# Performance work log

Hardware: AMD Instinct MI355X
Metric: run time of the kernel (lower is better)

Reference implementation:

```python
import jax, jax.numpy as jnp
import numpy as np

GN_EPS = 1e-5
NN_EPS = 1e-8


def _three_nn_interpolate(xyz1, xyz2, points2):
    # xyz1: (B,N,3), xyz2: (B,M,3), points2: (B,M,C) -> (B,N,C)
    src_sq = jnp.sum(xyz1 ** 2, axis=-1, keepdims=True)          # (B,N,1)
    dst_sq = jnp.sum(xyz2 ** 2, axis=-1)[:, None, :]             # (B,1,M)
    inner = jnp.einsum('bnd,bmd->bnm', xyz1, xyz2)               # (B,N,M)
    dist = src_sq - 2.0 * inner + dst_sq                         # (B,N,M)
    neg_d, idx = jax.lax.top_k(-dist, 3)                         # (B,N,3)
    d = -neg_d
    inv = 1.0 / (d + NN_EPS)
    w = inv / jnp.sum(inv, axis=-1, keepdims=True)               # (B,N,3)
    grouped = jax.vmap(lambda p, i: p[i])(points2, idx)          # (B,N,3,C)
    return jnp.sum(grouped * w[..., None], axis=2)               # (B,N,C)


def _group_norm(x, weight, bias, groups):
    # x: (B,C,N)
    B, C, N = x.shape
    xg = x.reshape(B, groups, C // groups, N)
    mu = jnp.mean(xg, axis=(2, 3), keepdims=True)
    var = jnp.var(xg, axis=(2, 3), keepdims=True)
    xg = (xg - mu) * jax.lax.rsqrt(var + GN_EPS)
    x = xg.reshape(B, C, N)
    return x * weight[None, :, None] + bias[None, :, None]


def setup_inputs() -> dict:
    key = jax.random.key(0)
    ks = jax.random.split(key, 10)
    B, N, M, C1, C2 = 8, 8192, 2048, 128, 256
    mlp = [256, 128]
    in_ch = C1 + C2
    inp = {
        'xyz1': jax.random.normal(ks[0], (B, N, 3), dtype=jnp.float32),
        'xyz2': jax.random.normal(ks[1], (B, M, 3), dtype=jnp.float32),
        'points1': jax.random.normal(ks[2], (B, N, C1), dtype=jnp.float32),
        'points2': jax.random.normal(ks[3], (B, M, C2), dtype=jnp.float32),
        'w0': jax.random.normal(ks[4], (mlp[0], in_ch), dtype=jnp.float32) * (1.0 / np.sqrt(in_ch)),
        'w1': jax.random.normal(ks[5], (mlp[1], mlp[0]), dtype=jnp.float32) * (1.0 / np.sqrt(mlp[0])),
        'gn0_w': jnp.ones((mlp[0],), dtype=jnp.float32),
        'gn0_b': jnp.zeros((mlp[0],), dtype=jnp.float32),
        'gn1_w': jnp.ones((mlp[1],), dtype=jnp.float32),
        'gn1_b': jnp.zeros((mlp[1],), dtype=jnp.float32),
    }
    return inp


def reference(xyz1, xyz2, points1, points2, w0, w1, gn0_w, gn0_b, gn1_w, gn1_b):
    interpolated = _three_nn_interpolate(xyz1, xyz2, points2)    # (B,N,C2)
    feat = jnp.concatenate([points1, interpolated], axis=-1)     # (B,N,C1+C2)
    # conv1d kernel size 1 == pointwise matmul; work in (B,C,N) layout for GN
    h = jnp.einsum('bnc,oc->bon', feat, w0)                      # (B,256,N)
    h = jax.nn.relu(_group_norm(h, gn0_w, gn0_b, groups=min(32, w0.shape[0])))
    h = jnp.einsum('bcn,oc->bon', h, w1)                         # (B,128,N)
    h = jax.nn.relu(_group_norm(h, gn1_w, gn1_b, groups=min(32, w1.shape[0])))
    return jnp.transpose(h, (0, 2, 1))                           # (B,N,128)
```

## Files before the change

### kernel.cpp

```cpp
#include <hip/hip_runtime.h>


#define DEVI __device__ __forceinline__

static constexpr int B  = 8;
static constexpr int N  = 8192;
static constexpr int M  = 2048;
static constexpr int C1 = 128;
static constexpr int C2 = 256;
static constexpr int CIN = C1 + C2;
static constexpr int H0 = 256;
static constexpr int H1 = 128;
static constexpr int BN = B * N;
static constexpr int NSEG = 8;
static constexpr int SEGL = M / NSEG;

typedef __bf16 bf16x8 __attribute__((ext_vector_type(8)));
typedef float  f32x4  __attribute__((ext_vector_type(4)));
typedef unsigned short ushort8v __attribute__((ext_vector_type(8)));

DEVI float bf2f(unsigned short u) {
    union { unsigned int i; float f; } v; v.i = ((unsigned int)u) << 16; return v.f;
}
DEVI unsigned short f2bf(float f) {
    union { float f; unsigned int i; } v; v.f = f;
    unsigned int x = v.i;
    return (unsigned short)((x + 0x7fffu + ((x >> 16) & 1u)) >> 16);
}
DEVI float ldin(const void* p, size_t i, int bf) {
    return bf ? bf2f(((const unsigned short*)p)[i]) : ((const float*)p)[i];
}
DEVI void ld8(const void* p, size_t i, int bf, float r[8]) {
    if (bf) {
        const ushort8v u = *(const ushort8v*)((const unsigned short*)p + i);
#pragma unroll
        for (int k = 0; k < 8; k++) r[k] = bf2f(u[k]);
    } else {
        const float4 a = *(const float4*)((const float*)p + i);
        const float4 b = *(const float4*)((const float*)p + i + 4);
        r[0] = a.x; r[1] = a.y; r[2] = a.z; r[3] = a.w;
        r[4] = b.x; r[5] = b.y; r[6] = b.z; r[7] = b.w;
    }
}

DEVI void gload16(const void* g, void* l) {
    __builtin_amdgcn_global_load_lds(
        (const __attribute__((address_space(1))) void*)g,
        (__attribute__((address_space(3))) void*)l, 16, 0, 0);
}

__global__ __launch_bounds__(64) void detect_dtype_kernel(const void* __restrict__ xyz1,
                                                          int* __restrict__ flag)
{
    const unsigned short* u = (const unsigned short*)xyz1;
    const int lane = threadIdx.x;
    const float av = fabsf(bf2f(u[2 * lane]));
    const bool in_range = (av >= 1e-4f && av <= 100.0f);
    const unsigned long long m = __ballot(in_range);
    if (lane == 0) flag[0] = (__popcll(m) >= 32) ? 1 : 0;
}

__global__ __launch_bounds__(256) void prep_kernel(
    const void* __restrict__ w0, const void* __restrict__ w1,
    const void* __restrict__ xyz2,
    unsigned short* __restrict__ w0b, unsigned short* __restrict__ w1b,
    float4* __restrict__ c4, float* __restrict__ partz,
    const int* __restrict__ flag)
{
    const int bf = flag[0];
    const int n0 = H0 * CIN;
    const int n1 = H1 * H0;
    const int n2 = B * M;
    const int n3 = 1024;
    const int total = n0 + n1 + n2 + n3;
    for (int i = blockIdx.x * blockDim.x + threadIdx.x; i < total; i += gridDim.x * blockDim.x) {
        if (i < n0) {
            w0b[i] = bf ? ((const unsigned short*)w0)[i] : f2bf(((const float*)w0)[i]);
        } else if (i < n0 + n1) {
            const int j = i - n0;
            w1b[j] = bf ? ((const unsigned short*)w1)[j] : f2bf(((const float*)w1)[j]);
        } else if (i < n0 + n1 + n2) {
            const int j = i - n0 - n1;
            const float x = ldin(xyz2, (size_t)j * 3 + 0, bf);
            const float y = ldin(xyz2, (size_t)j * 3 + 1, bf);
            const float z = ldin(xyz2, (size_t)j * 3 + 2, bf);
            const float sq = __fadd_rn(__fadd_rn(__fmul_rn(x, x), __fmul_rn(y, y)), __fmul_rn(z, z));
            c4[j] = make_float4(x, y, z, 0.5f * sq);
        } else {
            partz[i - n0 - n1 - n2] = 0.f;
        }
    }
}

__global__ __launch_bounds__(256) void knn3_split_kernel(
    const void* __restrict__ xyz1, const float4* __restrict__ c4,
    int* __restrict__ ci, const int* __restrict__ flag)
{
    const int bf = flag[0];
    const int tid = threadIdx.x;
    const int gid = blockIdx.x * 256 + tid;
    const int s = blockIdx.y;
    const int b = __builtin_amdgcn_readfirstlane(gid >> 13);

    const float x1 = ldin(xyz1, (size_t)gid * 3 + 0, bf);
    const float y1 = ldin(xyz1, (size_t)gid * 3 + 1, bf);
    const float z1 = ldin(xyz1, (size_t)gid * 3 + 2, bf);

    const float4* __restrict__ cand = c4 + b * M + s * SEGL;
    const int jbase = s * SEGL;
    constexpr int HALF = SEGL / 2;

    float a0 = 3.4e38f, a1 = 3.4e38f, a2 = 3.4e38f;
    int   ia0 = 0, ia1 = 0, ia2 = 0;
    float g0 = 3.4e38f, g1 = 3.4e38f, g2 = 3.4e38f;
    int   ig0 = 0, ig1 = 0, ig2 = 0;

#pragma unroll 4
    for (int j = 0; j < HALF; ++j) {
        const float4 pA = cand[j];
        const float4 pB = cand[j + HALF];
        const float sA = __builtin_fmaf(-x1, pA.x,
                          __builtin_fmaf(-y1, pA.y,
                           __builtin_fmaf(-z1, pA.z, pA.w)));
        const float sB = __builtin_fmaf(-x1, pB.x,
                          __builtin_fmaf(-y1, pB.y,
                           __builtin_fmaf(-z1, pB.z, pB.w)));
        {
            const int jn = jbase + j;
            const bool c0 = sA < a0;
            const float t1 = fmaxf(sA, a0); a0 = fminf(sA, a0);
            const int  tj1 = c0 ? ia0 : jn; ia0 = c0 ? jn : ia0;
            const bool c1 = t1 < a1;
            const float t2 = fmaxf(t1, a1); a1 = fminf(t1, a1);
            const int  tj2 = c1 ? ia1 : tj1; ia1 = c1 ? tj1 : ia1;
            const bool c2 = t2 < a2;
            a2 = fminf(t2, a2); ia2 = c2 ? tj2 : ia2;
        }
        {
            const int jn = jbase + HALF + j;
            const bool c0 = sB < g0;
            const float t1 = fmaxf(sB, g0); g0 = fminf(sB, g0);
            const int  tj1 = c0 ? ig0 : jn; ig0 = c0 ? jn : ig0;
            const bool c1 = t1 < g1;
            const float t2 = fmaxf(t1, g1); g1 = fminf(t1, g1);
            const int  tj2 = c1 ? ig1 : tj1; ig1 = c1 ? tj1 : ig1;
            const bool c2 = t2 < g2;
            g2 = fminf(t2, g2); ig2 = c2 ? tj2 : ig2;
        }
    }

    float mv[3] = { g0, g1, g2 };
    int   mi[3] = { ig0, ig1, ig2 };
#pragma unroll
    for (int k = 0; k < 3; ++k) {
        const float sv = mv[k]; const int jn = mi[k];
        const bool c0 = sv < a0;
        const float t1 = fmaxf(sv, a0); a0 = fminf(sv, a0);
        const int  tj1 = c0 ? ia0 : jn; ia0 = c0 ? jn : ia0;
        const bool c1 = t1 < a1;
        const float t2 = fmaxf(t1, a1); a1 = fminf(t1, a1);
        const int  tj2 = c1 ? ia1 : tj1; ia1 = c1 ? tj1 : ia1;
        const bool c2 = t2 < a2;
        a2 = fminf(t2, a2); ia2 = c2 ? tj2 : ia2;
    }

    ci[(size_t)(s * 3 + 0) * BN + gid] = ia0;
    ci[(size_t)(s * 3 + 1) * BN + gid] = ia1;
    ci[(size_t)(s * 3 + 2) * BN + gid] = ia2;
}

__global__ __launch_bounds__(256) void knn3_merge_kernel(
    const void* __restrict__ xyz1, const float4* __restrict__ c4,
    const int* __restrict__ ci,
    int* __restrict__ nn_idx, float* __restrict__ nn_w,
    const int* __restrict__ flag)
{
    const int bf = flag[0];
    const int gid = blockIdx.x * 256 + threadIdx.x;
    const int b = gid >> 13;

    const float x1 = ldin(xyz1, (size_t)gid * 3 + 0, bf);
    const float y1 = ldin(xyz1, (size_t)gid * 3 + 1, bf);
    const float z1 = ldin(xyz1, (size_t)gid * 3 + 2, bf);
    const float sq1 = __fadd_rn(__fadd_rn(__fmul_rn(x1, x1), __fmul_rn(y1, y1)), __fmul_rn(z1, z1));

    float bd0 = 3.4e38f, bd1 = 3.4e38f, bd2 = 3.4e38f;
    int   bi0 = 0x7fffffff, bi1 = 0x7fffffff, bi2 = 0x7fffffff;

#pragma unroll
    for (int k = 0; k < 3 * NSEG; ++k) {
        const int ix = ci[(size_t)k * BN + gid];
        const float4 p = c4[b * M + ix];
        const float inner = __fadd_rn(__fadd_rn(__fmul_rn(x1, p.x), __fmul_rn(y1, p.y)),
                                      __fmul_rn(z1, p.z));
        const float pw2 = p.w + p.w;
        const float d = __fadd_rn(__fsub_rn(sq1, __fmul_rn(2.0f, inner)), pw2);
        const bool lt2 = (d < bd2) || (d == bd2 && ix < bi2);
        if (lt2) {
            const bool lt0 = (d < bd0) || (d == bd0 && ix < bi0);
            const bool lt1 = (d < bd1) || (d == bd1 && ix < bi1);
            if (lt0)      { bd2 = bd1; bi2 = bi1; bd1 = bd0; bi1 = bi0; bd0 = d; bi0 = ix; }
            else if (lt1) { bd2 = bd1; bi2 = bi1; bd1 = d; bi1 = ix; }
            else          { bd2 = d; bi2 = ix; }
        }
    }

    const float v0 = 1.0f / (bd0 + 1e-8f);
    const float v1 = 1.0f / (bd1 + 1e-8f);
    const float v2 = 1.0f / (bd2 + 1e-8f);
    const float s = v0 + v1 + v2;
    nn_idx[gid * 3 + 0] = bi0; nn_idx[gid * 3 + 1] = bi1; nn_idx[gid * 3 + 2] = bi2;
    nn_w[gid * 3 + 0] = v0 / s; nn_w[gid * 3 + 1] = v1 / s; nn_w[gid * 3 + 2] = v2 / s;
}

__global__ __launch_bounds__(256, 2) void gemm1_kernel(
    const void* __restrict__ p1, const void* __restrict__ p2,
    const int* __restrict__ nn_idx, const float* __restrict__ nn_w,
    const unsigned short* __restrict__ W,
    unsigned short* __restrict__ h0, float2* __restrict__ part,
    const int* __restrict__ flag)
{
    constexpr int K = CIN;
    constexpr int COUT = H0;
    __shared__ __align__(16) char lds[49152];

    const int bf = flag[0];
    const int tid = threadIdx.x;
    const int l   = tid & 63;
    const int w   = tid >> 6;
    const int rowBase = blockIdx.x * 128;
    const int b = rowBase >> 13;

    const int srow  = l >> 3;
    const int sslot = l & 7;

    int arow[4]; int aidx[4][3]; float aw[4][3];
#pragma unroll
    for (int i = 0; i < 4; i++) {
        const int r = (w * 4 + i) * 8 + srow;
        arow[i] = r;
        const int p = rowBase + r;
#pragma unroll
        for (int k = 0; k < 3; k++) {
            aidx[i][k] = nn_idx[p * 3 + k];
            aw[i][k]   = nn_w[p * 3 + k];
        }
    }

    f32x4 acc[4][8];
#pragma unroll
    for (int i = 0; i < 4; i++)
#pragma unroll
        for (int j = 0; j < 8; j++) acc[i][j] = (f32x4)0.0f;

    const int wr  = (tid >> 7) & 1;
    const int wc  = (tid >> 6) & 1;
    const int rl  = l & 15;
    const int kq  = l >> 4;
    const int swz = (l & 7) << 4;
    int aoff[4], boff[8];
#pragma unroll
    for (int i = 0; i < 4; i++) aoff[i] = (wr * 64 + i * 16 + rl) * 128;
#pragma unroll
    for (int j = 0; j < 8; j++) boff[j] = 16384 + (wc * 128 + j * 16 + rl) * 128;

    constexpr int NT = K / 64;

#pragma unroll 1
    for (int t = 0; t < NT; ++t) {
        const int k0 = t * 64;
#pragma unroll
        for (int i = 0; i < 8; ++i) {
            const int cb = w * 8 + i;
            const int r  = cb * 8 + srow;
            const int ke = (sslot ^ (r & 7)) << 3;
            gload16(W + ((size_t)r * K + k0 + ke), lds + 16384 + cb * 1024);
        }
#pragma unroll
        for (int i = 0; i < 4; ++i) {
            const int r = arow[i];
            const int kslot = sslot ^ (r & 7);
            const int c = k0 + (kslot << 3);
            float v[8];
            if (k0 < C1) {
                ld8(p1, (size_t)(rowBase + r) * C1 + c, bf, v);
            } else {
                const int c2 = c - C1;
                float t0[8], t1[8], t2[8];
                ld8(p2, (size_t)(b * M + aidx[i][0]) * C2 + c2, bf, t0);
                ld8(p2, (size_t)(b * M + aidx[i][1]) * C2 + c2, bf, t1);
                ld8(p2, (size_t)(b * M + aidx[i][2]) * C2 + c2, bf, t2);
                const float w0v = aw[i][0], w1v = aw[i][1], w2v = aw[i][2];
#pragma unroll
                for (int k = 0; k < 8; k++) v[k] = w0v * t0[k] + w1v * t1[k] + w2v * t2[k];
            }
            ushort8v o;
#pragma unroll
            for (int k = 0; k < 8; k++) o[k] = f2bf(v[k]);
            *(ushort8v*)(lds + r * 128 + (sslot << 4)) = o;
        }
        __syncthreads();
#pragma unroll
        for (int ks = 0; ks < 2; ++ks) {
            const int kb = (ks * 64 + kq * 16) ^ swz;
            bf16x8 af[4], bfr[8];
#pragma unroll
            for (int i = 0; i < 4; i++) af[i]  = *(const bf16x8*)(lds + aoff[i] + kb);
#pragma unroll
            for (int j = 0; j < 8; j++) bfr[j] = *(const bf16x8*)(lds + boff[j] + kb);
#pragma unroll
            for (int i = 0; i < 4; i++)
#pragma unroll
                for (int j = 0; j < 8; j++)
                    acc[i][j] = __builtin_amdgcn_mfma_f32_16x16x32_bf16(af[i], bfr[j], acc[i][j], 0, 0, 0);
        }
        __syncthreads();
    }

    const int crow = rowBase + wr * 64 + kq * 4;
    const int ccol = wc * 128 + rl;
    float gsum[8], gss[8];
#pragma unroll
    for (int j = 0; j < 8; j++) {
        float s = 0.f, ss = 0.f;
#pragma unroll
        for (int i = 0; i < 4; i++)
#pragma unroll
            for (int r = 0; r < 4; r++) {
                const unsigned short hb = f2bf(acc[i][j][r]);
                h0[(size_t)(crow + i * 16 + r) * COUT + ccol + j * 16] = hb;
                const float x = bf2f(hb);
                s += x; ss += x * x;
            }
        gsum[j] = s; gss[j] = ss;
    }
    __syncthreads();
    float2* sred = (float2*)lds;
    if (tid < 32) sred[tid] = make_float2(0.f, 0.f);
    __syncthreads();
#pragma unroll
    for (int j = 0; j < 8; j++) {
        const int g = wc * 16 + j * 2 + (rl >> 3);
        atomicAdd(&sred[g].x, gsum[j]);
        atomicAdd(&sred[g].y, gss[j]);
    }
    __syncthreads();
    if (tid < 32) {
        atomicAdd(&part[b * 32 + tid].x, sred[tid].x);
        atomicAdd(&part[b * 32 + tid].y, sred[tid].y);
    }
}

__global__ __launch_bounds__(256) void gemm2_kernel(
    const unsigned short* __restrict__ h0, const float2* __restrict__ st0,
    const void* __restrict__ gw, const void* __restrict__ gb,
    const unsigned short* __restrict__ W,
    unsigned short* __restrict__ h1, float2* __restrict__ part,
    const int* __restrict__ flag)
{
    constexpr int K = H0;
    constexpr int COUT = H1;
    __shared__ __align__(16) char lds[32768];

    const int bf = flag[0];
    const int tid = threadIdx.x;
    const int l   = tid & 63;
    const int w   = tid >> 6;
    const int rowBase = blockIdx.x * 128;
    const int b = rowBase >> 13;

    const int srow  = l >> 3;
    const int sslot = l & 7;

    f32x4 acc[4][4];
#pragma unroll
    for (int i = 0; i < 4; i++)
#pragma unroll
        for (int j = 0; j < 4; j++) acc[i][j] = (f32x4)0.0f;

    const int wr  = (tid >> 7) & 1;
    const int wc  = (tid >> 6) & 1;
    const int rl  = l & 15;
    const int kq  = l >> 4;
    const int swz = (l & 7) << 4;
    int aoff[4], boff[4];
#pragma unroll
    for (int i = 0; i < 4; i++) {
        aoff[i] = (wr * 64 + i * 16 + rl) * 128;
        boff[i] = 16384 + (wc * 64 + i * 16 + rl) * 128;
    }

    constexpr int NT = K / 64;

#pragma unroll 1
    for (int t = 0; t < NT; ++t) {
        const int k0 = t * 64;
#pragma unroll
        for (int i = 0; i < 4; ++i) {
            const int cb = w * 4 + i;
            const int r  = cb * 8 + srow;
            const int ke = (sslot ^ (r & 7)) << 3;
            gload16(W + ((size_t)r * K + k0 + ke), lds + 16384 + cb * 1024);
        }
#pragma unroll
        for (int i = 0; i < 4; ++i) {
            const int r = (w * 4 + i) * 8 + srow;
            const int kslot = sslot ^ (r & 7);
            const int c = k0 + (kslot << 3);
            const float2 ms = st0[b * 32 + (c >> 3)];
            float gwv[8], gbv[8];
            ld8(gw, c, bf, gwv);
            ld8(gb, c, bf, gbv);
            const ushort8v hv = *(const ushort8v*)(h0 + (size_t)(rowBase + r) * H0 + c);
            ushort8v o;
#pragma unroll
            for (int k = 0; k < 8; k++) {
                const float x = bf2f(hv[k]);
                o[k] = f2bf(fmaxf((x - ms.x) * ms.y * gwv[k] + gbv[k], 0.f));
            }
            *(ushort8v*)(lds + r * 128 + (sslot << 4)) = o;
        }
        __syncthreads();
#pragma unroll
        for (int ks = 0; ks < 2; ++ks) {
            const int kb = (ks * 64 + kq * 16) ^ swz;
            bf16x8 af[4], bfr[4];
#pragma unroll
            for (int i = 0; i < 4; i++) af[i]  = *(const bf16x8*)(lds + aoff[i] + kb);
#pragma unroll
            for (int j = 0; j < 4; j++) bfr[j] = *(const bf16x8*)(lds + boff[j] + kb);
#pragma unroll
            for (int i = 0; i < 4; i++)
#pragma unroll
                for (int j = 0; j < 4; j++)
                    acc[i][j] = __builtin_amdgcn_mfma_f32_16x16x32_bf16(af[i], bfr[j], acc[i][j], 0, 0, 0);
        }
        __syncthreads();
    }

    const int crow = rowBase + wr * 64 + kq * 4;
    const int ccol = wc * 64 + rl;
    float gsum[4], gss[4];
#pragma unroll
    for (int j = 0; j < 4; j++) {
        float s = 0.f, ss = 0.f;
#pragma unroll
        for (int i = 0; i < 4; i++)
#pragma unroll
            for (int r = 0; r < 4; r++) {
                const unsigned short hb = f2bf(acc[i][j][r]);
                h1[(size_t)(crow + i * 16 + r) * COUT + ccol + j * 16] = hb;
                const float x = bf2f(hb);
                s += x; ss += x * x;
            }
        gsum[j] = s; gss[j] = ss;
    }
    __syncthreads();
    float2* sred = (float2*)lds;
    if (tid < 32) sred[tid] = make_float2(0.f, 0.f);
    __syncthreads();
#pragma unroll
    for (int j = 0; j < 4; j++) {
        const int g = wc * 16 + j * 4 + (rl >> 2);
        atomicAdd(&sred[g].x, gsum[j]);
        atomicAdd(&sred[g].y, gss[j]);
    }
    __syncthreads();
    if (tid < 32) {
        atomicAdd(&part[b * 32 + tid].x, sred[tid].x);
        atomicAdd(&part[b * 32 + tid].y, sred[tid].y);
    }
}

__global__ __launch_bounds__(256) void gn_finalize_kernel(
    const float2* __restrict__ part, float2* __restrict__ st, float cnt)
{
    const int t = threadIdx.x;
    const float2 p = part[t];
    const float mu  = p.x / cnt;
    const float var = p.y / cnt - mu * mu;
    st[t] = make_float2(mu, rsqrtf(var + 1e-5f));
}

__global__ __launch_bounds__(256) void gn_norm_relu_kernel(
    const unsigned short* __restrict__ h, const float2* __restrict__ st,
    const void* __restrict__ gw, const void* __restrict__ gb,
    void* __restrict__ out, int C, int cpg, int total4,
    const int* __restrict__ flag)
{
    const int bf = flag[0];
    const int C4 = C >> 2;
    for (int i4 = blockIdx.x * blockDim.x + threadIdx.x; i4 < total4; i4 += gridDim.x * blockDim.x) {
        const int c = (i4 % C4) * 4;
        const int p = i4 / C4;
        const int b = p >> 13;
        const float2 ms = st[b * (C / cpg) + c / cpg];
        const ushort4 hv = *(const ushort4*)(h + (size_t)i4 * 4);
        float r[4] = { bf2f(hv.x), bf2f(hv.y), bf2f(hv.z), bf2f(hv.w) };
#pragma unroll
        for (int k = 0; k < 4; k++) {
            const float gwv = ldin(gw, c + k, bf);
            const float gbv = ldin(gb, c + k, bf);
            r[k] = fmaxf((r[k] - ms.x) * ms.y * gwv + gbv, 0.f);
        }
        if (bf) {
            ushort4 o;
            o.x = f2bf(r[0]); o.y = f2bf(r[1]); o.z = f2bf(r[2]); o.w = f2bf(r[3]);
            *(ushort4*)((unsigned short*)out + (size_t)i4 * 4) = o;
        } else {
            float4 o; o.x = r[0]; o.y = r[1]; o.z = r[2]; o.w = r[3];
            *(float4*)((float*)out + (size_t)i4 * 4) = o;
        }
    }
}

extern "C" void kernel_launch(void* const* d_in, const int* in_sizes, int n_in,
                              void* d_out, int out_size, void* d_ws, size_t ws_size,
                              hipStream_t stream)
{
    const void* xyz1    = d_in[0];
    const void* xyz2    = d_in[1];
    const void* points1 = d_in[2];
    const void* points2 = d_in[3];
    const void* w0      = d_in[4];
    const void* w1      = d_in[5];
    const void* gn0w    = d_in[6];
    const void* gn0b    = d_in[7];
    const void* gn1w    = d_in[8];
    const void* gn1b    = d_in[9];

    char* ws = (char*)d_ws;
    int*            nn_idx = (int*)ws;
    float*          nn_w   = (float*)(ws + 786432);
    unsigned short* h0     = (unsigned short*)(ws + 1572864);
    unsigned short* h1     = (unsigned short*)(ws + 35127296);
    unsigned short* w0b    = (unsigned short*)(ws + 51904512);
    unsigned short* w1b    = (unsigned short*)(ws + 52101120);
    float2*         st0    = (float2*)(ws + 52166656);
    float2*         st1    = (float2*)(ws + 52168704);
    int*            flag   = (int*)(ws + 52170752);
    float4*         c4     = (float4*)(ws + 52170816);
    int*            ci     = (int*)(ws + 52432960);
    float2*         part0  = (float2*)(ws + 58724416);
    float2*         part1  = (float2*)(ws + 58726464);

    detect_dtype_kernel<<<1, 64, 0, stream>>>(xyz1, flag);

    prep_kernel<<<576, 256, 0, stream>>>(w0, w1, xyz2, w0b, w1b, c4, (float*)part0, flag);

    {
        dim3 g(BN / 256, NSEG);
        knn3_split_kernel<<<g, 256, 0, stream>>>(xyz1, c4, ci, flag);
    }
    knn3_merge_kernel<<<BN / 256, 256, 0, stream>>>(xyz1, c4, ci, nn_idx, nn_w, flag);

    gemm1_kernel<<<BN / 128, 256, 0, stream>>>(points1, points2, nn_idx, nn_w,
                                               w0b, h0, part0, flag);
    gn_finalize_kernel<<<1, 256, 0, stream>>>(part0, st0, (float)N * (H0 / 32));

    gemm2_kernel<<<BN / 128, 256, 0, stream>>>(h0, st0, gn0w, gn0b, w1b, h1, part1, flag);
    gn_finalize_kernel<<<1, 256, 0, stream>>>(part1, st1, (float)N * (H1 / 32));

    gn_norm_relu_kernel<<<1024, 256, 0, stream>>>(h1, st1, gn1w, gn1b, d_out,
                                                  H1, H1 / 32, BN * H1 / 4, flag);
}
```

Baseline: 353.7 us.

## Split interpolation out of GEMM1 into a bf16 feature buffer and retile GEMM1

Converts points1 and points2 to bf16 in the prep kernel. A new kernel gathers the three neighbours, interpolates them and writes a concatenated bf16 feature matrix. GEMM1 then loads both its A and B tiles through global_load_lds with 512 threads and 4x4 MFMA tiles per wave, instead of doing gathers inside its K loop. This removes the irregular gather latency from the matmul, but adds a round trip of the ~50MB feature buffer through memory and extra conversion traffic.

```diff
diff --git a/kernel.cpp b/kernel.cpp
--- a/kernel.cpp
+++ b/kernel.cpp
@@ -42,6 +42,11 @@
         r[4] = b.x; r[5] = b.y; r[6] = b.z; r[7] = b.w;
     }
 }
+DEVI void ld8b(const unsigned short* p, size_t i, float r[8]) {
+    const ushort8v u = *(const ushort8v*)(p + i);
+#pragma unroll
+    for (int k = 0; k < 8; k++) r[k] = bf2f(u[k]);
+}
 
 DEVI void gload16(const void* g, void* l) {
     __builtin_amdgcn_global_load_lds(
@@ -60,35 +65,56 @@
     if (lane == 0) flag[0] = (__popcll(m) >= 32) ? 1 : 0;
 }
 
+DEVI void cvt8(const void* src, unsigned short* dst, size_t j8, int bf) {
+    if (bf) {
+        *(ushort8v*)(dst + j8 * 8) = *(const ushort8v*)((const unsigned short*)src + j8 * 8);
+    } else {
+        float r[8];
+        ld8(src, j8 * 8, 0, r);
+        ushort8v o;
+#pragma unroll
+        for (int k = 0; k < 8; k++) o[k] = f2bf(r[k]);
+        *(ushort8v*)(dst + j8 * 8) = o;
+    }
+}
+
 __global__ __launch_bounds__(256) void prep_kernel(
     const void* __restrict__ w0, const void* __restrict__ w1,
+    const void* __restrict__ p1, const void* __restrict__ p2,
     const void* __restrict__ xyz2,
     unsigned short* __restrict__ w0b, unsigned short* __restrict__ w1b,
+    unsigned short* __restrict__ pb1, unsigned short* __restrict__ pb2,
     float4* __restrict__ c4, float* __restrict__ partz,
     const int* __restrict__ flag)
 {
     const int bf = flag[0];
-    const int n0 = H0 * CIN;
-    const int n1 = H1 * H0;
-    const int n2 = B * M;
-    const int n3 = 1024;
-    const int total = n0 + n1 + n2 + n3;
-    for (int i = blockIdx.x * blockDim.x + threadIdx.x; i < total; i += gridDim.x * blockDim.x) {
-        if (i < n0) {
-            w0b[i] = bf ? ((const unsigned short*)w0)[i] : f2bf(((const float*)w0)[i]);
-        } else if (i < n0 + n1) {
-            const int j = i - n0;
-            w1b[j] = bf ? ((const unsigned short*)w1)[j] : f2bf(((const float*)w1)[j]);
-        } else if (i < n0 + n1 + n2) {
-            const int j = i - n0 - n1;
+    constexpr int R0 = H0 * CIN / 8;
+    constexpr int R1 = H1 * H0 / 8;
+    constexpr int R2 = B * M;
+    constexpr int R3 = BN * C1 / 8;
+    constexpr int R4 = B * M * C2 / 8;
+    constexpr int R5 = 1024;
+    constexpr int TOT = R0 + R1 + R2 + R3 + R4 + R5;
+    for (int i = blockIdx.x * blockDim.x + threadIdx.x; i < TOT; i += gridDim.x * blockDim.x) {
+        int j = i;
+        if (j < R0) { cvt8(w0, w0b, j, bf); continue; }
+        j -= R0;
+        if (j < R1) { cvt8(w1, w1b, j, bf); continue; }
+        j -= R1;
+        if (j < R2) {
             const float x = ldin(xyz2, (size_t)j * 3 + 0, bf);
             const float y = ldin(xyz2, (size_t)j * 3 + 1, bf);
             const float z = ldin(xyz2, (size_t)j * 3 + 2, bf);
             const float sq = __fadd_rn(__fadd_rn(__fmul_rn(x, x), __fmul_rn(y, y)), __fmul_rn(z, z));
             c4[j] = make_float4(x, y, z, 0.5f * sq);
-        } else {
-            partz[i - n0 - n1 - n2] = 0.f;
-        }
+            continue;
+        }
+        j -= R2;
+        if (j < R3) { cvt8(p1, pb1, j, bf); continue; }
+        j -= R3;
+        if (j < R4) { cvt8(p2, pb2, j, bf); continue; }
+        j -= R4;
+        partz[j] = 0.f;
     }
 }
 
@@ -213,18 +239,47 @@
     nn_w[gid * 3 + 0] = v0 / s; nn_w[gid * 3 + 1] = v1 / s; nn_w[gid * 3 + 2] = v2 / s;
 }
 
-__global__ __launch_bounds__(256, 2) void gemm1_kernel(
-    const void* __restrict__ p1, const void* __restrict__ p2,
+__global__ __launch_bounds__(256) void interp_concat_kernel(
+    const unsigned short* __restrict__ pb1, const unsigned short* __restrict__ pb2,
     const int* __restrict__ nn_idx, const float* __restrict__ nn_w,
+    unsigned short* __restrict__ feat)
+{
+    const int total = BN * (CIN / 8);
+    for (int idx = blockIdx.x * blockDim.x + threadIdx.x; idx < total; idx += gridDim.x * blockDim.x) {
+        const int c8 = idx % 48;
+        const int p  = idx / 48;
+        const int c  = c8 * 8;
+        if (c < C1) {
+            *(ushort8v*)(feat + (size_t)idx * 8) =
+                *(const ushort8v*)(pb1 + (size_t)p * C1 + c);
+        } else {
+            const int b  = p >> 13;
+            const int c2 = c - C1;
+            const int*   id = nn_idx + p * 3;
+            const float* wv = nn_w  + p * 3;
+            float t0[8], t1[8], t2[8];
+            ld8b(pb2, (size_t)(b * M + id[0]) * C2 + c2, t0);
+            ld8b(pb2, (size_t)(b * M + id[1]) * C2 + c2, t1);
+            ld8b(pb2, (size_t)(b * M + id[2]) * C2 + c2, t2);
+            const float w0v = wv[0], w1v = wv[1], w2v = wv[2];
+            ushort8v o;
+#pragma unroll
+            for (int k = 0; k < 8; k++)
+                o[k] = f2bf(w0v * t0[k] + w1v * t1[k] + w2v * t2[k]);
+            *(ushort8v*)(feat + (size_t)idx * 8) = o;
+        }
+    }
+}
+
+__global__ __launch_bounds__(512) void gemm1_kernel(
+    const unsigned short* __restrict__ A,
     const unsigned short* __restrict__ W,
-    unsigned short* __restrict__ h0, float2* __restrict__ part,
-    const int* __restrict__ flag)
+    unsigned short* __restrict__ h0, float2* __restrict__ part)
 {
     constexpr int K = CIN;
     constexpr int COUT = H0;
     __shared__ __align__(16) char lds[49152];
 
-    const int bf = flag[0];
     const int tid = threadIdx.x;
     const int l   = tid & 63;
     const int w   = tid >> 6;
@@ -234,35 +289,23 @@
     const int srow  = l >> 3;
     const int sslot = l & 7;
 
-    int arow[4]; int aidx[4][3]; float aw[4][3];
-#pragma unroll
-    for (int i = 0; i < 4; i++) {
-        const int r = (w * 4 + i) * 8 + srow;
-        arow[i] = r;
-        const int p = rowBase + r;
-#pragma unroll
-        for (int k = 0; k < 3; k++) {
-            aidx[i][k] = nn_idx[p * 3 + k];
-            aw[i][k]   = nn_w[p * 3 + k];
-        }
-    }
-
-    f32x4 acc[4][8];
+    f32x4 acc[4][4];
 #pragma unroll
     for (int i = 0; i < 4; i++)
 #pragma unroll
-        for (int j = 0; j < 8; j++) acc[i][j] = (f32x4)0.0f;
-
-    const int wr  = (tid >> 7) & 1;
-    const int wc  = (tid >> 6) & 1;
+        for (int j = 0; j < 4; j++) acc[i][j] = (f32x4)0.0f;
+
+    const int wr  = w >> 2;
+    const int wc  = w & 3;
     const int rl  = l & 15;
     const int kq  = l >> 4;
     const int swz = (l & 7) << 4;
-    int aoff[4], boff[8];
-#pragma unroll
-    for (int i = 0; i < 4; i++) aoff[i] = (wr * 64 + i * 16 + rl) * 128;
-#pragma unroll
-    for (int j = 0; j < 8; j++) boff[j] = 16384 + (wc * 128 + j * 16 + rl) * 128;
+    int aoff[4], boff[4];
+#pragma unroll
+    for (int i = 0; i < 4; i++) {
+        aoff[i] = (wr * 64 + i * 16 + rl) * 128;
+        boff[i] = 16384 + (wc * 64 + i * 16 + rl) * 128;
+    }
 
     constexpr int NT = K / 64;
 
@@ -270,58 +313,41 @@
     for (int t = 0; t < NT; ++t) {
         const int k0 = t * 64;
 #pragma unroll
-        for (int i = 0; i < 8; ++i) {
-            const int cb = w * 8 + i;
-            const int r  = cb * 8 + srow;
-            const int ke = (sslot ^ (r & 7)) << 3;
-            gload16(W + ((size_t)r * K + k0 + ke), lds + 16384 + cb * 1024);
-        }
-#pragma unroll
-        for (int i = 0; i < 4; ++i) {
-            const int r = arow[i];
-            const int kslot = sslot ^ (r & 7);
-            const int c = k0 + (kslot << 3);
-            float v[8];
-            if (k0 < C1) {
-                ld8(p1, (size_t)(rowBase + r) * C1 + c, bf, v);
+        for (int i = 0; i < 6; ++i) {
+            const int ch = w * 6 + i;
+            if (ch < 16) {
+                const int r  = ch * 8 + srow;
+                const int ke = (sslot ^ (r & 7)) << 3;
+                gload16(A + ((size_t)(rowBase + r) * K + k0 + ke), lds + ch * 1024);
             } else {
-                const int c2 = c - C1;
-                float t0[8], t1[8], t2[8];
-                ld8(p2, (size_t)(b * M + aidx[i][0]) * C2 + c2, bf, t0);
-                ld8(p2, (size_t)(b * M + aidx[i][1]) * C2 + c2, bf, t1);
-                ld8(p2, (size_t)(b * M + aidx[i][2]) * C2 + c2, bf, t2);
-                const float w0v = aw[i][0], w1v = aw[i][1], w2v = aw[i][2];
-#pragma unroll
-                for (int k = 0; k < 8; k++) v[k] = w0v * t0[k] + w1v * t1[k] + w2v * t2[k];
+                const int rb = (ch - 16) * 8 + srow;
+                const int ke = (sslot ^ (rb & 7)) << 3;
+                gload16(W + ((size_t)rb * K + k0 + ke), lds + 16384 + (ch - 16) * 1024);
             }
-            ushort8v o;
-#pragma unroll
-            for (int k = 0; k < 8; k++) o[k] = f2bf(v[k]);
-            *(ushort8v*)(lds + r * 128 + (sslot << 4)) = o;
         }
         __syncthreads();
 #pragma unroll
         for (int ks = 0; ks < 2; ++ks) {
             const int kb = (ks * 64 + kq * 16) ^ swz;
-            bf16x8 af[4], bfr[8];
+            bf16x8 af[4], bfr[4];
 #pragma unroll
             for (int i = 0; i < 4; i++) af[i]  = *(const bf16x8*)(lds + aoff[i] + kb);
 #pragma unroll
-            for (int j = 0; j < 8; j++) bfr[j] = *(const bf16x8*)(lds + boff[j] + kb);
+            for (int j = 0; j < 4; j++) bfr[j] = *(const bf16x8*)(lds + boff[j] + kb);
 #pragma unroll
             for (int i = 0; i < 4; i++)
 #pragma unroll
-                for (int j = 0; j < 8; j++)
+                for (int j = 0; j < 4; j++)
                     acc[i][j] = __builtin_amdgcn_mfma_f32_16x16x32_bf16(af[i], bfr[j], acc[i][j], 0, 0, 0);
         }
         __syncthreads();
     }
 
     const int crow = rowBase + wr * 64 + kq * 4;
-    const int ccol = wc * 128 + rl;
-    float gsum[8], gss[8];
-#pragma unroll
-    for (int j = 0; j < 8; j++) {
+    const int ccol = wc * 64 + rl;
+    float gsum[4], gss[4];
+#pragma unroll
+    for (int j = 0; j < 4; j++) {
         float s = 0.f, ss = 0.f;
 #pragma unroll
         for (int i = 0; i < 4; i++)
@@ -339,8 +365,8 @@
     if (tid < 32) sred[tid] = make_float2(0.f, 0.f);
     __syncthreads();
 #pragma unroll
-    for (int j = 0; j < 8; j++) {
-        const int g = wc * 16 + j * 2 + (rl >> 3);
+    for (int j = 0; j < 4; j++) {
+        const int g = wc * 8 + j * 2 + (rl >> 3);
         atomicAdd(&sred[g].x, gsum[j]);
         atomicAdd(&sred[g].y, gss[j]);
     }
@@ -532,21 +558,25 @@
     char* ws = (char*)d_ws;
     int*            nn_idx = (int*)ws;
     float*          nn_w   = (float*)(ws + 786432);
-    unsigned short* h0     = (unsigned short*)(ws + 1572864);
-    unsigned short* h1     = (unsigned short*)(ws + 35127296);
-    unsigned short* w0b    = (unsigned short*)(ws + 51904512);
-    unsigned short* w1b    = (unsigned short*)(ws + 52101120);
-    float2*         st0    = (float2*)(ws + 52166656);
-    float2*         st1    = (float2*)(ws + 52168704);
-    int*            flag   = (int*)(ws + 52170752);
-    float4*         c4     = (float4*)(ws + 52170816);
-    int*            ci     = (int*)(ws + 52432960);
-    float2*         part0  = (float2*)(ws + 58724416);
-    float2*         part1  = (float2*)(ws + 58726464);
+    unsigned short* feat   = (unsigned short*)(ws + 1572864);
+    unsigned short* h1     = feat;
+    unsigned short* h0     = (unsigned short*)(ws + 51904512);
+    unsigned short* w0b    = (unsigned short*)(ws + 85458944);
+    unsigned short* w1b    = (unsigned short*)(ws + 85655552);
+    unsigned short* pb1    = (unsigned short*)(ws + 85721088);
+    unsigned short* pb2    = (unsigned short*)(ws + 102498304);
+    float4*         c4     = (float4*)(ws + 110886912);
+    int*            ci     = (int*)(ws + 111149056);
+    float2*         part0  = (float2*)(ws + 117440512);
+    float2*         part1  = (float2*)(ws + 117442560);
+    float2*         st0    = (float2*)(ws + 117444608);
+    float2*         st1    = (float2*)(ws + 117446656);
+    int*            flag   = (int*)(ws + 117448704);
 
     detect_dtype_kernel<<<1, 64, 0, stream>>>(xyz1, flag);
 
-    prep_kernel<<<576, 256, 0, stream>>>(w0, w1, xyz2, w0b, w1b, c4, (float*)part0, flag);
+    prep_kernel<<<2048, 256, 0, stream>>>(w0, w1, points1, points2, xyz2,
+                                          w0b, w1b, pb1, pb2, c4, (float*)part0, flag);
 
     {
         dim3 g(BN / 256, NSEG);
@@ -554,8 +584,9 @@
     }
     knn3_merge_kernel<<<BN / 256, 256, 0, stream>>>(xyz1, c4, ci, nn_idx, nn_w, flag);
 
-    gemm1_kernel<<<BN / 128, 256, 0, stream>>>(points1, points2, nn_idx, nn_w,
-                                               w0b, h0, part0, flag);
+    interp_concat_kernel<<<2048, 256, 0, stream>>>(pb1, pb2, nn_idx, nn_w, feat);
+
+    gemm1_kernel<<<BN / 128, 512, 0, stream>>>(feat, w0b, h0, part0);
     gn_finalize_kernel<<<1, 256, 0, stream>>>(part0, st0, (float)N * (H0 / 32));
 
     gemm2_kernel<<<BN / 128, 256, 0, stream>>>(h0, st0, gn0w, gn0b, w1b, h1, part1, flag);
```

Measured after the change: 303.9 us. 1.16x faster.
